# Optimization experiments

Measured on AMD Instinct MI355X. Metric: run time of the kernel, lower is better.

The kernel has to match this reference:

```python
import jax, jax.numpy as jnp
import numpy as np

N = 16384
RANK = 10
IN_F = 64
OUT_F = 64


def setup_inputs() -> dict:
    key = jax.random.key(0)
    k1, k2, k3, k4, k5 = jax.random.split(key, 5)
    return {
        "x": jax.random.normal(k1, (N, IN_F), dtype=jnp.float32),
        "source_embed": jax.random.normal(k2, (N, RANK), dtype=jnp.float32),
        "target_embed": jax.random.normal(k3, (RANK, N), dtype=jnp.float32),
        "W": jax.random.normal(k4, (OUT_F, IN_F), dtype=jnp.float32) * 0.1,
        "b": jax.random.normal(k5, (OUT_F,), dtype=jnp.float32) * 0.1,
    }


def reference(x, source_embed, target_embed, W, b):
    # Learned adjacency: [N, N] = softmax(relu(source @ target), row-wise)
    scores = jax.nn.relu(source_embed @ target_embed)  # [N, N]
    adj = jax.nn.softmax(scores, axis=1)               # [N, N]
    # Graph conv then linear (torch Linear: x @ W.T + b)
    agg = adj @ x                                       # [N, IN_F]
    return agg @ W.T + b                                # [N, OUT_F]
```

## Files before the change

kernel.cpp:

```cpp
#include <hip/hip_runtime.h>
#include <hip/hip_bf16.h>


constexpr int N    = 16384;
constexpr int RANK = 10;
constexpr int F    = 64;
constexpr int NH   = N / 2;

typedef float f32x4 __attribute__((ext_vector_type(4)));
typedef short bf16x8 __attribute__((ext_vector_type(8)));

static __device__ __forceinline__ unsigned short f2bf_rne(float f) {
    union { float f; unsigned int u; } a; a.f = f;
    unsigned int u = a.u;
    u += 0x7FFFu + ((u >> 16) & 1u);
    return (unsigned short)(u >> 16);
}
static __device__ __forceinline__ float bf2f(unsigned short h) {
    union { unsigned int u; float f; } a; a.u = ((unsigned int)h) << 16;
    return a.f;
}

__global__ __launch_bounds__(256)
void prep_te(const float* __restrict__ te, uint4* __restrict__ tefrag, int jt0) {
    const int tid  = threadIdx.x;
    const int lt   = blockIdx.x * 4 + (tid >> 6);
    const int jt   = jt0 + lt;
    const int lane = tid & 63;
    const int g = lane >> 4, il = lane & 15;
    union { unsigned short us[8]; uint4 v; } pk;
#pragma unroll
    for (int b = 0; b < 8; ++b) {
        const int k = 8 * g + b;
        unsigned short o = 0;
        if (k < 30) {
            const int band = (k < 10) ? 0 : (k < 20 ? 1 : 2);
            const int r = k - band * 10;
            const float v = te[r * N + jt * 16 + il];
            const unsigned short h = f2bf_rne(v);
            o = (band == 2) ? f2bf_rne(v - bf2f(h)) : h;
        }
        pk.us[b] = o;
    }
    tefrag[lt * 64 + lane] = pk.v;
}

__global__ __launch_bounds__(256)
void prep_y(const float* __restrict__ x, const float* __restrict__ W,
            uint4* __restrict__ yfrag, int js0) {
    __shared__ float xs[32][68];
    const int jl  = blockIdx.x;
    const int js  = js0 + jl;
    const int tid = threadIdx.x;
#pragma unroll
    for (int i = 0; i < 2; ++i) {
        const int fi = tid * 2 + i;
        const int r = fi >> 4, c4 = fi & 15;
        const float4 v = *reinterpret_cast<const float4*>(x + (size_t)(js * 32 + r) * F + c4 * 4);
        *reinterpret_cast<float4*>(&xs[r][c4 * 4]) = v;
    }
    __syncthreads();
    const int t = tid >> 6, lane = tid & 63;
    const int g = lane >> 4, il = lane & 15;
    const int f = t * 16 + il;
    float y[8];
#pragma unroll
    for (int b = 0; b < 8; ++b) y[b] = 0.f;
    const float* wr = W + f * F;
#pragma unroll
    for (int k4 = 0; k4 < F / 4; ++k4) {
        const float4 wv = *reinterpret_cast<const float4*>(wr + 4 * k4);
#pragma unroll
        for (int b = 0; b < 8; ++b) {
            const int row = 16 * (b >> 2) + 4 * g + (b & 3);
            const float4 xv = *reinterpret_cast<const float4*>(&xs[row][4 * k4]);
            y[b] = fmaf(xv.x, wv.x, y[b]);
            y[b] = fmaf(xv.y, wv.y, y[b]);
            y[b] = fmaf(xv.z, wv.z, y[b]);
            y[b] = fmaf(xv.w, wv.w, y[b]);
        }
    }
    union { unsigned short us[8]; uint4 v; } pk;
#pragma unroll
    for (int b = 0; b < 8; ++b) pk.us[b] = f2bf_rne(y[b]);
    yfrag[(jl * 4 + t) * 64 + lane] = pk.v;
}

__global__ __launch_bounds__(512, 4)
void gcn_main(const float* __restrict__ se, const uint4* __restrict__ tefrag,
              const uint4* __restrict__ yfrag, const float* __restrict__ bias,
              float* __restrict__ out, float* __restrict__ lsum_self,
              const float* __restrict__ lsum_other, int phase) {
    const int tid  = threadIdx.x;
    const int lane = tid & 63;
    const int wave = tid >> 6;
    const int g = lane >> 4, il = lane & 15;
    const int rowbase = blockIdx.x << 5;

    bf16x8 sef[2];
#pragma unroll
    for (int rt = 0; rt < 2; ++rt) {
        union { short s8[8]; bf16x8 v; } pk;
        const int row = rowbase + rt * 16 + il;
#pragma unroll
        for (int b = 0; b < 8; ++b) {
            const int k = 8 * g + b;
            unsigned short o = 0;
            if (k < 30) {
                const int band = (k < 10) ? 0 : (k < 20 ? 1 : 2);
                const int r = k - band * 10;
                const float v = se[row * RANK + r];
                const unsigned short h = f2bf_rne(v);
                o = (band == 1) ? f2bf_rne(v - bf2f(h)) : h;
            }
            pk.s8[b] = (short)o;
        }
        sef[rt] = pk.v;
    }

    f32x4 acc[2][4];
#pragma unroll
    for (int rt = 0; rt < 2; ++rt)
#pragma unroll
        for (int ft = 0; ft < 4; ++ft) acc[rt][ft] = f32x4{0.f, 0.f, 0.f, 0.f};
    float lsum0 = 0.f, lsum1 = 0.f;

    const uint4* tb = tefrag + (size_t)wave * 64 * 64 + lane;
    const uint4* yb = yfrag + (size_t)wave * 32 * 256 + lane;

    for (int s = 0; s < 32; ++s) {
        const uint4 ta0 = tb[0];
        const uint4 ta1 = tb[64];
        const f32x4 z = {0.f, 0.f, 0.f, 0.f};
        f32x4 sc00 = __builtin_amdgcn_mfma_f32_16x16x32_bf16(__builtin_bit_cast(bf16x8, ta0), sef[0], z, 0, 0, 0);
        f32x4 sc01 = __builtin_amdgcn_mfma_f32_16x16x32_bf16(__builtin_bit_cast(bf16x8, ta1), sef[0], z, 0, 0, 0);
        f32x4 sc10 = __builtin_amdgcn_mfma_f32_16x16x32_bf16(__builtin_bit_cast(bf16x8, ta0), sef[1], z, 0, 0, 0);
        f32x4 sc11 = __builtin_amdgcn_mfma_f32_16x16x32_bf16(__builtin_bit_cast(bf16x8, ta1), sef[1], z, 0, 0, 0);

        union { short s8[8]; bf16x8 v; } af0, af1;
#pragma unroll
        for (int q = 0; q < 4; ++q) {
            const float p00 = __expf(fmaxf(sc00[q], 0.f));
            const float p01 = __expf(fmaxf(sc01[q], 0.f));
            const float p10 = __expf(fmaxf(sc10[q], 0.f));
            const float p11 = __expf(fmaxf(sc11[q], 0.f));
            lsum0 += p00 + p01;
            lsum1 += p10 + p11;
            af0.s8[q]     = (short)__builtin_bit_cast(unsigned short, __float2bfloat16(p00));
            af0.s8[4 + q] = (short)__builtin_bit_cast(unsigned short, __float2bfloat16(p01));
            af1.s8[q]     = (short)__builtin_bit_cast(unsigned short, __float2bfloat16(p10));
            af1.s8[4 + q] = (short)__builtin_bit_cast(unsigned short, __float2bfloat16(p11));
        }

        const uint4 y0 = yb[0];
        const uint4 y1 = yb[64];
        acc[0][0] = __builtin_amdgcn_mfma_f32_16x16x32_bf16(af0.v, __builtin_bit_cast(bf16x8, y0), acc[0][0], 0, 0, 0);
        acc[1][0] = __builtin_amdgcn_mfma_f32_16x16x32_bf16(af1.v, __builtin_bit_cast(bf16x8, y0), acc[1][0], 0, 0, 0);
        acc[0][1] = __builtin_amdgcn_mfma_f32_16x16x32_bf16(af0.v, __builtin_bit_cast(bf16x8, y1), acc[0][1], 0, 0, 0);
        acc[1][1] = __builtin_amdgcn_mfma_f32_16x16x32_bf16(af1.v, __builtin_bit_cast(bf16x8, y1), acc[1][1], 0, 0, 0);
        const uint4 y2 = yb[128];
        const uint4 y3 = yb[192];
        acc[0][2] = __builtin_amdgcn_mfma_f32_16x16x32_bf16(af0.v, __builtin_bit_cast(bf16x8, y2), acc[0][2], 0, 0, 0);
        acc[1][2] = __builtin_amdgcn_mfma_f32_16x16x32_bf16(af1.v, __builtin_bit_cast(bf16x8, y2), acc[1][2], 0, 0, 0);
        acc[0][3] = __builtin_amdgcn_mfma_f32_16x16x32_bf16(af0.v, __builtin_bit_cast(bf16x8, y3), acc[0][3], 0, 0, 0);
        acc[1][3] = __builtin_amdgcn_mfma_f32_16x16x32_bf16(af1.v, __builtin_bit_cast(bf16x8, y3), acc[1][3], 0, 0, 0);

        tb += 128;
        yb += 256;
    }

    lsum0 += __shfl_xor(lsum0, 16); lsum0 += __shfl_xor(lsum0, 32);
    lsum1 += __shfl_xor(lsum1, 16); lsum1 += __shfl_xor(lsum1, 32);

    __shared__ float s_acc[4][2048];
    __shared__ float s_l[8][32];

    if (g == 0) { s_l[wave][il] = lsum0; s_l[wave][16 + il] = lsum1; }

    if (wave < 4) {
#pragma unroll
        for (int rt = 0; rt < 2; ++rt)
#pragma unroll
            for (int ft = 0; ft < 4; ++ft)
#pragma unroll
                for (int q = 0; q < 4; ++q)
                    s_acc[wave][(rt * 16 + 4 * g + q) * 64 + ft * 16 + il] = acc[rt][ft][q];
    }
    __syncthreads();
    if (wave >= 4) {
#pragma unroll
        for (int rt = 0; rt < 2; ++rt)
#pragma unroll
            for (int ft = 0; ft < 4; ++ft)
#pragma unroll
                for (int q = 0; q < 4; ++q) {
                    const int a = (rt * 16 + 4 * g + q) * 64 + ft * 16 + il;
                    s_acc[wave - 4][a] += acc[rt][ft][q];
                }
    }
    __syncthreads();

    const int idx  = tid << 2;
    const int row  = idx >> 6;
    const int feat = idx & 63;
    f32x4 v = {0.f, 0.f, 0.f, 0.f};
#pragma unroll
    for (int w = 0; w < 4; ++w) v = v + *reinterpret_cast<const f32x4*>(&s_acc[w][idx]);
    float ls = 0.f;
#pragma unroll
    for (int w = 0; w < 8; ++w) ls += s_l[w][row];

    const int orow = rowbase + row;
    float* op = out + (size_t)orow * F + feat;

    if (phase == 0) {
        if (feat == 0) lsum_self[orow] = ls;
        float4 o; o.x = v[0]; o.y = v[1]; o.z = v[2]; o.w = v[3];
        *reinterpret_cast<float4*>(op) = o;
    } else {
        const float4 prev = *reinterpret_cast<const float4*>(op);
        const float lst = ls + lsum_other[orow];
        const float inv = 1.f / lst;
        const float4 bv = *reinterpret_cast<const float4*>(bias + feat);
        float4 o;
        o.x = (v[0] + prev.x) * inv + bv.x;
        o.y = (v[1] + prev.y) * inv + bv.y;
        o.z = (v[2] + prev.z) * inv + bv.z;
        o.w = (v[3] + prev.w) * inv + bv.w;
        *reinterpret_cast<float4*>(op) = o;
    }
}

extern "C" void kernel_launch(void* const* d_in, const int* in_sizes, int n_in,
                              void* d_out, int out_size, void* d_ws, size_t ws_size,
                              hipStream_t stream) {
    const float* x  = (const float*)d_in[0];
    const float* se = (const float*)d_in[1];
    const float* te = (const float*)d_in[2];
    const float* W  = (const float*)d_in[3];
    const float* b  = (const float*)d_in[4];
    float* out = (float*)d_out;

    uint4* tefrag = (uint4*)d_ws;
    uint4* yfrag  = (uint4*)((char*)d_ws + (512u << 10));
    float* lsumA  = (float*)((char*)d_ws + (1536u << 10));
    float* lsumB  = lsumA + N;

    prep_te<<<NH / 16 / 4, 256, 0, stream>>>(te, tefrag, 0);
    prep_y <<<NH / 32,     256, 0, stream>>>(x, W, yfrag, 0);
    gcn_main<<<N / 32, 512, 0, stream>>>(se, tefrag, yfrag, b, out, lsumA, lsumB, 0);

    prep_te<<<NH / 16 / 4, 256, 0, stream>>>(te, tefrag, NH / 16);
    prep_y <<<NH / 32,     256, 0, stream>>>(x, W, yfrag, NH / 32);
    gcn_main<<<N / 32, 512, 0, stream>>>(se, tefrag, yfrag, b, out, lsumB, lsumA, 1);
}
```

Measured before the change: 167.8 us.

## Halve rows per block, use exp2 with prescaled scores, MFMA row sums, merged prep

```diff
diff --git a/kernel.cpp b/kernel.cpp
--- a/kernel.cpp
+++ b/kernel.cpp
@@ -1,5 +1,4 @@
 #include <hip/hip_runtime.h>
-#include <hip/hip_bf16.h>
 
 
 constexpr int N    = 16384;
@@ -10,83 +9,85 @@
 typedef float f32x4 __attribute__((ext_vector_type(4)));
 typedef short bf16x8 __attribute__((ext_vector_type(8)));
 
-static __device__ __forceinline__ unsigned short f2bf_rne(float f) {
-    union { float f; unsigned int u; } a; a.f = f;
-    unsigned int u = a.u;
-    u += 0x7FFFu + ((u >> 16) & 1u);
-    return (unsigned short)(u >> 16);
-}
-static __device__ __forceinline__ float bf2f(unsigned short h) {
-    union { unsigned int u; float f; } a; a.u = ((unsigned int)h) << 16;
-    return a.f;
+constexpr float LOG2E = 1.4426950408889634f;
+
+static __device__ __forceinline__ float fexp2(float x) {
+    float r;
+    asm("v_exp_f32 %0, %1" : "=v"(r) : "v"(x));
+    return r;
+}
+static __device__ __forceinline__ unsigned short bfbits(float f) {
+    return __builtin_bit_cast(unsigned short, (__bf16)f);
 }
 
 __global__ __launch_bounds__(256)
-void prep_te(const float* __restrict__ te, uint4* __restrict__ tefrag, int jt0) {
+void prep(const float* __restrict__ x, const float* __restrict__ W,
+          const float* __restrict__ te,
+          uint4* __restrict__ yfrag, uint4* __restrict__ tefrag,
+          int js0, int jt0)
+{
     const int tid  = threadIdx.x;
-    const int lt   = blockIdx.x * 4 + (tid >> 6);
-    const int jt   = jt0 + lt;
     const int lane = tid & 63;
     const int g = lane >> 4, il = lane & 15;
-    union { unsigned short us[8]; uint4 v; } pk;
-#pragma unroll
-    for (int b = 0; b < 8; ++b) {
-        const int k = 8 * g + b;
-        unsigned short o = 0;
-        if (k < 30) {
-            const int band = (k < 10) ? 0 : (k < 20 ? 1 : 2);
-            const int r = k - band * 10;
-            const float v = te[r * N + jt * 16 + il];
-            const unsigned short h = f2bf_rne(v);
-            o = (band == 2) ? f2bf_rne(v - bf2f(h)) : h;
-        }
-        pk.us[b] = o;
-    }
-    tefrag[lt * 64 + lane] = pk.v;
-}
-
-__global__ __launch_bounds__(256)
-void prep_y(const float* __restrict__ x, const float* __restrict__ W,
-            uint4* __restrict__ yfrag, int js0) {
-    __shared__ float xs[32][68];
-    const int jl  = blockIdx.x;
-    const int js  = js0 + jl;
-    const int tid = threadIdx.x;
-#pragma unroll
-    for (int i = 0; i < 2; ++i) {
-        const int fi = tid * 2 + i;
-        const int r = fi >> 4, c4 = fi & 15;
-        const float4 v = *reinterpret_cast<const float4*>(x + (size_t)(js * 32 + r) * F + c4 * 4);
-        *reinterpret_cast<float4*>(&xs[r][c4 * 4]) = v;
-    }
-    __syncthreads();
-    const int t = tid >> 6, lane = tid & 63;
-    const int g = lane >> 4, il = lane & 15;
-    const int f = t * 16 + il;
-    float y[8];
-#pragma unroll
-    for (int b = 0; b < 8; ++b) y[b] = 0.f;
-    const float* wr = W + f * F;
-#pragma unroll
-    for (int k4 = 0; k4 < F / 4; ++k4) {
-        const float4 wv = *reinterpret_cast<const float4*>(wr + 4 * k4);
+
+    if (blockIdx.x < 256) {
+        __shared__ float xs[32][68];
+        const int jl = blockIdx.x;
+        const int js = js0 + jl;
+#pragma unroll
+        for (int i = 0; i < 2; ++i) {
+            const int fi = tid * 2 + i;
+            const int r = fi >> 4, c4 = fi & 15;
+            const float4 v = *reinterpret_cast<const float4*>(x + (size_t)(js * 32 + r) * F + c4 * 4);
+            *reinterpret_cast<float4*>(&xs[r][c4 * 4]) = v;
+        }
+        __syncthreads();
+        const int t = tid >> 6;
+        const int f = t * 16 + il;
+        float y[8];
+#pragma unroll
+        for (int b = 0; b < 8; ++b) y[b] = 0.f;
+        const float* wr = W + f * F;
+#pragma unroll
+        for (int k4 = 0; k4 < F / 4; ++k4) {
+            const float4 wv = *reinterpret_cast<const float4*>(wr + 4 * k4);
+#pragma unroll
+            for (int b = 0; b < 8; ++b) {
+                const int row = 16 * (b >> 2) + 4 * g + (b & 3);
+                const float4 xv = *reinterpret_cast<const float4*>(&xs[row][4 * k4]);
+                y[b] = fmaf(xv.x, wv.x, y[b]);
+                y[b] = fmaf(xv.y, wv.y, y[b]);
+                y[b] = fmaf(xv.z, wv.z, y[b]);
+                y[b] = fmaf(xv.w, wv.w, y[b]);
+            }
+        }
+        union { unsigned short us[8]; uint4 v; } pk;
+#pragma unroll
+        for (int b = 0; b < 8; ++b) pk.us[b] = bfbits(y[b]);
+        yfrag[(jl * 4 + t) * 64 + lane] = pk.v;
+    } else {
+        const int lt = (blockIdx.x - 256) * 4 + (tid >> 6);
+        const int jt = jt0 + lt;
+        union { unsigned short us[8]; uint4 v; } pk;
 #pragma unroll
         for (int b = 0; b < 8; ++b) {
-            const int row = 16 * (b >> 2) + 4 * g + (b & 3);
-            const float4 xv = *reinterpret_cast<const float4*>(&xs[row][4 * k4]);
-            y[b] = fmaf(xv.x, wv.x, y[b]);
-            y[b] = fmaf(xv.y, wv.y, y[b]);
-            y[b] = fmaf(xv.z, wv.z, y[b]);
-            y[b] = fmaf(xv.w, wv.w, y[b]);
-        }
-    }
-    union { unsigned short us[8]; uint4 v; } pk;
-#pragma unroll
-    for (int b = 0; b < 8; ++b) pk.us[b] = f2bf_rne(y[b]);
-    yfrag[(jl * 4 + t) * 64 + lane] = pk.v;
-}
-
-__global__ __launch_bounds__(512, 4)
+            const int k = 8 * g + b;
+            unsigned short o = 0;
+            if (k < 30) {
+                const int band = (k < 10) ? 0 : (k < 20 ? 1 : 2);
+                const int r = k - band * 10;
+                const float v = te[r * N + jt * 16 + il];
+                const __bf16 hb = (__bf16)v;
+                o = (band == 2) ? bfbits(v - (float)hb)
+                                : __builtin_bit_cast(unsigned short, hb);
+            }
+            pk.us[b] = o;
+        }
+        tefrag[lt * 64 + lane] = pk.v;
+    }
+}
+
+__global__ __launch_bounds__(512, 8)
 void gcn_main(const float* __restrict__ se, const uint4* __restrict__ tefrag,
               const uint4* __restrict__ yfrag, const float* __restrict__ bias,
               float* __restrict__ out, float* __restrict__ lsum_self,
@@ -95,13 +96,12 @@
     const int lane = tid & 63;
     const int wave = tid >> 6;
     const int g = lane >> 4, il = lane & 15;
-    const int rowbase = blockIdx.x << 5;
-
-    bf16x8 sef[2];
-#pragma unroll
-    for (int rt = 0; rt < 2; ++rt) {
-        union { short s8[8]; bf16x8 v; } pk;
-        const int row = rowbase + rt * 16 + il;
+    const int rowbase = blockIdx.x << 4;
+
+    bf16x8 sef;
+    {
+        union { unsigned short us[8]; bf16x8 v; } pk;
+        const int row = rowbase + il;
 #pragma unroll
         for (int b = 0; b < 8; ++b) {
             const int k = 8 * g + b;
@@ -109,21 +109,25 @@
             if (k < 30) {
                 const int band = (k < 10) ? 0 : (k < 20 ? 1 : 2);
                 const int r = k - band * 10;
-                const float v = se[row * RANK + r];
-                const unsigned short h = f2bf_rne(v);
-                o = (band == 1) ? f2bf_rne(v - bf2f(h)) : h;
+                const float a = se[row * RANK + r] * LOG2E;
+                const __bf16 hb = (__bf16)a;
+                o = (band == 1) ? bfbits(a - (float)hb)
+                                : __builtin_bit_cast(unsigned short, hb);
             }
-            pk.s8[b] = (short)o;
-        }
-        sef[rt] = pk.v;
-    }
-
-    f32x4 acc[2][4];
-#pragma unroll
-    for (int rt = 0; rt < 2; ++rt)
-#pragma unroll
-        for (int ft = 0; ft < 4; ++ft) acc[rt][ft] = f32x4{0.f, 0.f, 0.f, 0.f};
-    float lsum0 = 0.f, lsum1 = 0.f;
+            pk.us[b] = o;
+        }
+        sef = pk.v;
+    }
+
+    union { unsigned short us[8]; bf16x8 v; } onesu;
+#pragma unroll
+    for (int b = 0; b < 8; ++b) onesu.us[b] = 0x3F80;
+    const bf16x8 ones = onesu.v;
+
+    f32x4 acc[4];
+#pragma unroll
+    for (int ft = 0; ft < 4; ++ft) acc[ft] = f32x4{0.f, 0.f, 0.f, 0.f};
+    f32x4 accL = {0.f, 0.f, 0.f, 0.f};
 
     const uint4* tb = tefrag + (size_t)wave * 64 * 64 + lane;
     const uint4* yb = yfrag + (size_t)wave * 32 * 256 + lane;
@@ -131,103 +135,87 @@
     for (int s = 0; s < 32; ++s) {
         const uint4 ta0 = tb[0];
         const uint4 ta1 = tb[64];
-        const f32x4 z = {0.f, 0.f, 0.f, 0.f};
-        f32x4 sc00 = __builtin_amdgcn_mfma_f32_16x16x32_bf16(__builtin_bit_cast(bf16x8, ta0), sef[0], z, 0, 0, 0);
-        f32x4 sc01 = __builtin_amdgcn_mfma_f32_16x16x32_bf16(__builtin_bit_cast(bf16x8, ta1), sef[0], z, 0, 0, 0);
-        f32x4 sc10 = __builtin_amdgcn_mfma_f32_16x16x32_bf16(__builtin_bit_cast(bf16x8, ta0), sef[1], z, 0, 0, 0);
-        f32x4 sc11 = __builtin_amdgcn_mfma_f32_16x16x32_bf16(__builtin_bit_cast(bf16x8, ta1), sef[1], z, 0, 0, 0);
-
-        union { short s8[8]; bf16x8 v; } af0, af1;
-#pragma unroll
-        for (int q = 0; q < 4; ++q) {
-            const float p00 = __expf(fmaxf(sc00[q], 0.f));
-            const float p01 = __expf(fmaxf(sc01[q], 0.f));
-            const float p10 = __expf(fmaxf(sc10[q], 0.f));
-            const float p11 = __expf(fmaxf(sc11[q], 0.f));
-            lsum0 += p00 + p01;
-            lsum1 += p10 + p11;
-            af0.s8[q]     = (short)__builtin_bit_cast(unsigned short, __float2bfloat16(p00));
-            af0.s8[4 + q] = (short)__builtin_bit_cast(unsigned short, __float2bfloat16(p01));
-            af1.s8[q]     = (short)__builtin_bit_cast(unsigned short, __float2bfloat16(p10));
-            af1.s8[4 + q] = (short)__builtin_bit_cast(unsigned short, __float2bfloat16(p11));
-        }
-
         const uint4 y0 = yb[0];
         const uint4 y1 = yb[64];
-        acc[0][0] = __builtin_amdgcn_mfma_f32_16x16x32_bf16(af0.v, __builtin_bit_cast(bf16x8, y0), acc[0][0], 0, 0, 0);
-        acc[1][0] = __builtin_amdgcn_mfma_f32_16x16x32_bf16(af1.v, __builtin_bit_cast(bf16x8, y0), acc[1][0], 0, 0, 0);
-        acc[0][1] = __builtin_amdgcn_mfma_f32_16x16x32_bf16(af0.v, __builtin_bit_cast(bf16x8, y1), acc[0][1], 0, 0, 0);
-        acc[1][1] = __builtin_amdgcn_mfma_f32_16x16x32_bf16(af1.v, __builtin_bit_cast(bf16x8, y1), acc[1][1], 0, 0, 0);
         const uint4 y2 = yb[128];
         const uint4 y3 = yb[192];
-        acc[0][2] = __builtin_amdgcn_mfma_f32_16x16x32_bf16(af0.v, __builtin_bit_cast(bf16x8, y2), acc[0][2], 0, 0, 0);
-        acc[1][2] = __builtin_amdgcn_mfma_f32_16x16x32_bf16(af1.v, __builtin_bit_cast(bf16x8, y2), acc[1][2], 0, 0, 0);
-        acc[0][3] = __builtin_amdgcn_mfma_f32_16x16x32_bf16(af0.v, __builtin_bit_cast(bf16x8, y3), acc[0][3], 0, 0, 0);
-        acc[1][3] = __builtin_amdgcn_mfma_f32_16x16x32_bf16(af1.v, __builtin_bit_cast(bf16x8, y3), acc[1][3], 0, 0, 0);
+
+        const f32x4 z = {0.f, 0.f, 0.f, 0.f};
+        const f32x4 sc0 = __builtin_amdgcn_mfma_f32_16x16x32_bf16(__builtin_bit_cast(bf16x8, ta0), sef, z, 0, 0, 0);
+        const f32x4 sc1 = __builtin_amdgcn_mfma_f32_16x16x32_bf16(__builtin_bit_cast(bf16x8, ta1), sef, z, 0, 0, 0);
+
+        union { __bf16 h[8]; bf16x8 v; } af;
+#pragma unroll
+        for (int q = 0; q < 4; ++q) {
+            const float p0 = fexp2(fmaxf(sc0[q], 0.f));
+            const float p1 = fexp2(fmaxf(sc1[q], 0.f));
+            af.h[q]     = (__bf16)p0;
+            af.h[4 + q] = (__bf16)p1;
+        }
+
+        acc[0] = __builtin_amdgcn_mfma_f32_16x16x32_bf16(af.v, __builtin_bit_cast(bf16x8, y0), acc[0], 0, 0, 0);
+        acc[1] = __builtin_amdgcn_mfma_f32_16x16x32_bf16(af.v, __builtin_bit_cast(bf16x8, y1), acc[1], 0, 0, 0);
+        acc[2] = __builtin_amdgcn_mfma_f32_16x16x32_bf16(af.v, __builtin_bit_cast(bf16x8, y2), acc[2], 0, 0, 0);
+        acc[3] = __builtin_amdgcn_mfma_f32_16x16x32_bf16(af.v, __builtin_bit_cast(bf16x8, y3), acc[3], 0, 0, 0);
+        accL   = __builtin_amdgcn_mfma_f32_16x16x32_bf16(af.v, ones, accL, 0, 0, 0);
 
         tb += 128;
         yb += 256;
     }
 
-    lsum0 += __shfl_xor(lsum0, 16); lsum0 += __shfl_xor(lsum0, 32);
-    lsum1 += __shfl_xor(lsum1, 16); lsum1 += __shfl_xor(lsum1, 32);
-
-    __shared__ float s_acc[4][2048];
-    __shared__ float s_l[8][32];
-
-    if (g == 0) { s_l[wave][il] = lsum0; s_l[wave][16 + il] = lsum1; }
-
+    __shared__ float s_acc[4][1024];
+    __shared__ float s_l[8][16];
+
+    if (il == 0) {
+#pragma unroll
+        for (int q = 0; q < 4; ++q) s_l[wave][4 * g + q] = accL[q];
+    }
     if (wave < 4) {
 #pragma unroll
-        for (int rt = 0; rt < 2; ++rt)
-#pragma unroll
-            for (int ft = 0; ft < 4; ++ft)
-#pragma unroll
-                for (int q = 0; q < 4; ++q)
-                    s_acc[wave][(rt * 16 + 4 * g + q) * 64 + ft * 16 + il] = acc[rt][ft][q];
+        for (int ft = 0; ft < 4; ++ft)
+#pragma unroll
+            for (int q = 0; q < 4; ++q)
+                s_acc[wave][(4 * g + q) * 64 + ft * 16 + il] = acc[ft][q];
     }
     __syncthreads();
     if (wave >= 4) {
 #pragma unroll
-        for (int rt = 0; rt < 2; ++rt)
-#pragma unroll
-            for (int ft = 0; ft < 4; ++ft)
-#pragma unroll
-                for (int q = 0; q < 4; ++q) {
-                    const int a = (rt * 16 + 4 * g + q) * 64 + ft * 16 + il;
-                    s_acc[wave - 4][a] += acc[rt][ft][q];
-                }
+        for (int ft = 0; ft < 4; ++ft)
+#pragma unroll
+            for (int q = 0; q < 4; ++q)
+                s_acc[wave - 4][(4 * g + q) * 64 + ft * 16 + il] += acc[ft][q];
     }
     __syncthreads();
 
-    const int idx  = tid << 2;
-    const int row  = idx >> 6;
-    const int feat = idx & 63;
-    f32x4 v = {0.f, 0.f, 0.f, 0.f};
-#pragma unroll
-    for (int w = 0; w < 4; ++w) v = v + *reinterpret_cast<const f32x4*>(&s_acc[w][idx]);
-    float ls = 0.f;
-#pragma unroll
-    for (int w = 0; w < 8; ++w) ls += s_l[w][row];
-
-    const int orow = rowbase + row;
-    float* op = out + (size_t)orow * F + feat;
-
-    if (phase == 0) {
-        if (feat == 0) lsum_self[orow] = ls;
-        float4 o; o.x = v[0]; o.y = v[1]; o.z = v[2]; o.w = v[3];
-        *reinterpret_cast<float4*>(op) = o;
-    } else {
-        const float4 prev = *reinterpret_cast<const float4*>(op);
-        const float lst = ls + lsum_other[orow];
-        const float inv = 1.f / lst;
-        const float4 bv = *reinterpret_cast<const float4*>(bias + feat);
-        float4 o;
-        o.x = (v[0] + prev.x) * inv + bv.x;
-        o.y = (v[1] + prev.y) * inv + bv.y;
-        o.z = (v[2] + prev.z) * inv + bv.z;
-        o.w = (v[3] + prev.w) * inv + bv.w;
-        *reinterpret_cast<float4*>(op) = o;
+    if (tid < 256) {
+        const int idx  = tid << 2;
+        const int row  = idx >> 6;
+        const int feat = idx & 63;
+        f32x4 v = {0.f, 0.f, 0.f, 0.f};
+#pragma unroll
+        for (int w = 0; w < 4; ++w) v = v + *reinterpret_cast<const f32x4*>(&s_acc[w][idx]);
+        float ls = 0.f;
+#pragma unroll
+        for (int w = 0; w < 8; ++w) ls += s_l[w][row];
+
+        const int orow = rowbase + row;
+        float* op = out + (size_t)orow * F + feat;
+
+        if (phase == 0) {
+            if (feat == 0) lsum_self[orow] = ls;
+            float4 o; o.x = v[0]; o.y = v[1]; o.z = v[2]; o.w = v[3];
+            *reinterpret_cast<float4*>(op) = o;
+        } else {
+            const float4 prev = *reinterpret_cast<const float4*>(op);
+            const float inv = 1.f / (ls + lsum_other[orow]);
+            const float4 bv = *reinterpret_cast<const float4*>(bias + feat);
+            float4 o;
+            o.x = (v[0] + prev.x) * inv + bv.x;
+            o.y = (v[1] + prev.y) * inv + bv.y;
+            o.z = (v[2] + prev.z) * inv + bv.z;
+            o.w = (v[3] + prev.w) * inv + bv.w;
+            *reinterpret_cast<float4*>(op) = o;
+        }
     }
 }
 
@@ -246,11 +234,9 @@
     float* lsumA  = (float*)((char*)d_ws + (1536u << 10));
     float* lsumB  = lsumA + N;
 
-    prep_te<<<NH / 16 / 4, 256, 0, stream>>>(te, tefrag, 0);
-    prep_y <<<NH / 32,     256, 0, stream>>>(x, W, yfrag, 0);
-    gcn_main<<<N / 32, 512, 0, stream>>>(se, tefrag, yfrag, b, out, lsumA, lsumB, 0);
-
-    prep_te<<<NH / 16 / 4, 256, 0, stream>>>(te, tefrag, NH / 16);
-    prep_y <<<NH / 32,     256, 0, stream>>>(x, W, yfrag, NH / 32);
-    gcn_main<<<N / 32, 512, 0, stream>>>(se, tefrag, yfrag, b, out, lsumB, lsumA, 1);
-}
+    prep<<<384, 256, 0, stream>>>(x, W, te, yfrag, tefrag, 0, 0);
+    gcn_main<<<N / 16, 512, 0, stream>>>(se, tefrag, yfrag, b, out, lsumA, lsumB, 0);
+
+    prep<<<384, 256, 0, stream>>>(x, W, te, yfrag, tefrag, NH / 32, NH / 16);
+    gcn_main<<<N / 16, 512, 0, stream>>>(se, tefrag, yfrag, b, out, lsumB, lsumA, 1);
+}
```

New measurement: 188.7 us. 12.5% more time.
